# Kernel tuning notes

Hardware: AMD Instinct MI355X
Metric: run time of the kernel (lower is better)

Reference implementation:

```python
import jax, jax.numpy as jnp
import numpy as np

N, T = 128, 20
E_IN, E_EMB, E_RNN = 2, 64, 256
N_IN, N_EMB, N_RNN, N_OUT = 2, 64, 128, 5
ATT = 64

# static edge index sets: diagonal = temporal edges (i,i), off-diagonal = spatial edges (i,j)
_DIAG = np.arange(N) * N + np.arange(N)
_OFFJ = np.array([[j for j in range(N) if j != i] for i in range(N)])  # [N, N-1]
_OFFD = (np.arange(N)[:, None] * N + _OFFJ).reshape(-1)               # [N*(N-1)]
_TEMP = (N - 1) / np.sqrt(ATT)  # attention temperature = num_edges / sqrt(attention_size)


def setup_inputs() -> dict:
    ks = iter(jax.random.split(jax.random.key(0), 40))
    def p(shape, s=0.05):
        return jax.random.normal(next(ks), shape, jnp.float32) * s
    return {
        "nodes": p((T, N, N_IN), 1.0),
        "edges": p((T, N * N, E_IN), 1.0),
        "h_edge0": jnp.zeros((N * N, E_RNN), jnp.float32),
        "c_edge0": jnp.zeros((N * N, E_RNN), jnp.float32),
        "h_node0": jnp.zeros((N, N_RNN), jnp.float32),
        "c_node0": jnp.zeros((N, N_RNN), jnp.float32),
        "t_enc_w": p((E_EMB, E_IN)), "t_enc_b": p((E_EMB,)),
        "t_wih": p((4 * E_RNN, E_EMB)), "t_whh": p((4 * E_RNN, E_RNN)),
        "t_bih": p((4 * E_RNN,)), "t_bhh": p((4 * E_RNN,)),
        "s_enc_w": p((E_EMB, E_IN)), "s_enc_b": p((E_EMB,)),
        "s_wih": p((4 * E_RNN, E_EMB)), "s_whh": p((4 * E_RNN, E_RNN)),
        "s_bih": p((4 * E_RNN,)), "s_bhh": p((4 * E_RNN,)),
        "att_t_w": p((ATT, E_RNN)), "att_t_b": p((ATT,)),
        "att_s_w": p((ATT, E_RNN)), "att_s_b": p((ATT,)),
        "n_enc_w": p((N_EMB, N_IN)), "n_enc_b": p((N_EMB,)),
        "n_attn_w": p((N_EMB, 2 * E_RNN)), "n_attn_b": p((N_EMB,)),
        "n_wih": p((4 * N_RNN, 2 * N_EMB)), "n_whh": p((4 * N_RNN, N_RNN)),
        "n_bih": p((4 * N_RNN,)), "n_bhh": p((4 * N_RNN,)),
        "out_w": p((N_OUT, N_RNN)), "out_b": p((N_OUT,)),
    }


def _lstm(x, h, c, wih, whh, bih, bhh):
    g = x @ wih.T + bih + h @ whh.T + bhh
    i, f, gg, o = jnp.split(g, 4, axis=-1)
    c2 = jax.nn.sigmoid(f) * c + jax.nn.sigmoid(i) * jnp.tanh(gg)
    return jax.nn.sigmoid(o) * jnp.tanh(c2), c2


def reference(nodes, edges, h_edge0, c_edge0, h_node0, c_node0,
              t_enc_w, t_enc_b, t_wih, t_whh, t_bih, t_bhh,
              s_enc_w, s_enc_b, s_wih, s_whh, s_bih, s_bhh,
              att_t_w, att_t_b, att_s_w, att_s_b,
              n_enc_w, n_enc_b, n_attn_w, n_attn_b,
              n_wih, n_whh, n_bih, n_bhh, out_w, out_b):
    def step(carry, xt):
        h_e, c_e, h_n, c_n = carry
        pos_t, edg_t = xt
        # temporal edge RNN on self edges (i,i)
        x_t = jax.nn.relu(edg_t[_DIAG] @ t_enc_w.T + t_enc_b)
        h_t, c_t = _lstm(x_t, h_e[_DIAG], c_e[_DIAG], t_wih, t_whh, t_bih, t_bhh)
        # spatial edge RNN on all pairwise edges (i,j), i != j
        x_s = jax.nn.relu(edg_t[_OFFD] @ s_enc_w.T + s_enc_b)
        h_s, c_s = _lstm(x_s, h_e[_OFFD], c_e[_OFFD], s_wih, s_whh, s_bih, s_bhh)
        h_e = h_e.at[_DIAG].set(h_t).at[_OFFD].set(h_s)
        c_e = c_e.at[_DIAG].set(c_t).at[_OFFD].set(c_s)
        # attention: each node attends over its N-1 spatial edge hidden states
        hs = h_s.reshape(N, N - 1, E_RNN)
        te = h_t @ att_t_w.T + att_t_b                          # [N, ATT]
        se = jnp.einsum('nkd,ad->nka', hs, att_s_w) + att_s_b   # [N, N-1, ATT]
        logits = jnp.einsum('nka,na->nk', se, te) * _TEMP
        w = jax.nn.softmax(logits, axis=-1)
        weighted = jnp.einsum('nk,nkd->nd', w, hs)              # [N, E_RNN]
        # node RNN
        enc = jax.nn.relu(pos_t @ n_enc_w.T + n_enc_b)
        h_edges = jnp.concatenate([h_t, weighted], axis=-1)
        h_emb = jax.nn.relu(h_edges @ n_attn_w.T + n_attn_b)
        h_n, c_n = _lstm(jnp.concatenate([enc, h_emb], axis=-1), h_n, c_n,
                         n_wih, n_whh, n_bih, n_bhh)
        out = h_n @ out_w.T + out_b
        return (h_e, c_e, h_n, c_n), out

    _, outs = jax.lax.scan(step, (h_edge0, c_edge0, h_node0, c_node0), (nodes, edges))
    return outs  # [T, N, 5]
```

## Files before the change

### kernel.cpp

```cpp
#include <hip/hip_runtime.h>
#include <cmath>

#define NN 128
#define TT 20
#define ERNN 256
#define TEMPSC 15.875f

typedef __attribute__((ext_vector_type(8))) short bf16x8;
typedef __attribute__((ext_vector_type(4))) float f32x4;

__device__ __forceinline__ float sigm(float x){ return 1.f/(1.f+__expf(-x)); }
__device__ __forceinline__ float ftanh(float x){ float e = __expf(2.f*x); return 1.f - 2.f/(e + 1.f); }
__device__ __forceinline__ float b2f(unsigned short u){ union{unsigned int i; float f;} v; v.i = ((unsigned int)u)<<16; return v.f; }
__device__ __forceinline__ unsigned short f2b(float x){ union{float f; unsigned int u;} v; v.f = x; unsigned int r = v.u + 0x7fffu + ((v.u>>16)&1u); return (unsigned short)(r>>16); }

typedef __attribute__((address_space(3))) unsigned int lds_u32;
typedef __attribute__((address_space(1))) unsigned int glb_u32;
__device__ __forceinline__ void glds16(const void* g, void* l){
    __builtin_amdgcn_global_load_lds((const glb_u32*)g, (lds_u32*)l, 16, 0, 0);
}

__device__ __forceinline__ size_t hoff(int r, int d){
    return ((size_t)((r>>7)*32 + (d>>3))*128 + (r&127))*8 + (d&7);
}

__global__ void k_prep_w2(const float* __restrict__ s_wih, const float* __restrict__ s_whh,
                          unsigned short* __restrict__ s_wHi,
                          const float* __restrict__ t_wih, const float* __restrict__ t_whh,
                          unsigned short* __restrict__ t_wHi){
    int idx = blockIdx.x*256 + threadIdx.x;
    if (idx >= 2*1024*320) return;
    int which = idx >= 1024*320;
    if (which) idx -= 1024*320;
    const float* wih = which ? t_wih : s_wih;
    const float* whh = which ? t_whh : s_whh;
    unsigned short* wHi = which ? t_wHi : s_wHi;
    int c = idx / 320, k = idx - c*320;
    int ch = ((c>>6)<<4) + (c&15), g = (c>>4)&3;
    int r = g*256 + ch;
    float v = (k < 64) ? wih[r*64 + k] : whh[r*256 + (k-64)];
    size_t dst = ((size_t)((c>>7)*40 + (k>>3))*128 + (c&127))*8 + (k&7);
    wHi[dst] = f2b(v);
}

__global__ void k_prep_small(const float* __restrict__ s_bih, const float* __restrict__ s_bhh,
                             float* __restrict__ s_bs,
                             const float* __restrict__ t_bih, const float* __restrict__ t_bhh,
                             float* __restrict__ t_bs,
                             const float* __restrict__ n_wih, const float* __restrict__ n_whh,
                             float* __restrict__ n_wT,
                             const float* __restrict__ n_bih, const float* __restrict__ n_bhh,
                             float* __restrict__ n_bs){
    int i = blockIdx.x*256 + threadIdx.x;
    if (i < 2048) {
        int c = i, which = c >= 1024;
        if (which) c -= 1024;
        const float* bih = which ? t_bih : s_bih;
        const float* bhh = which ? t_bhh : s_bhh;
        float* bs = which ? t_bs : s_bs;
        int ch = ((c>>6)<<4)+(c&15), g=(c>>4)&3;
        int r = g*256+ch;
        bs[c] = bih[r] + bhh[r];
    } else if (i < 2048 + 65536) {
        int j = i - 2048;
        int r = j >> 7, c = j & 127;
        n_wT[c*512 + r] = n_wih[j];
    } else if (i < 2048 + 131072) {
        int j = i - 2048 - 65536;
        int r = j >> 7, c = j & 127;
        n_wT[(128 + c)*512 + r] = n_whh[j];
    } else if (i < 2048 + 131072 + 512) {
        int j = i - 2048 - 131072;
        n_bs[j] = n_bih[j] + n_bhh[j];
    }
}

__global__ void k_prep_xenc(const float* __restrict__ edges,
                            const float* __restrict__ s_enc_w, const float* __restrict__ s_enc_b,
                            const float* __restrict__ t_enc_w, const float* __restrict__ t_enc_b,
                            unsigned short* __restrict__ xe){
    size_t g = (size_t)blockIdx.x*256 + threadIdx.x;
    if (g >= (size_t)TT*16384*8) return;
    int row = (int)(g & 127);
    size_t rest = g >> 7;
    int kc = (int)(rest & 7);
    int tile = (int)((rest >> 3) & 127);
    int t = (int)(rest >> 10);
    int r = tile*128 + row;
    bool sp = (r < 16256);
    int row_ij;
    if (sp) { int i = r/127, jj = r - i*127; row_ij = i*NN + jj + (jj>=i ? 1:0); }
    else    { row_ij = (r - 16256)*(NN+1); }
    const float* w = sp ? s_enc_w : t_enc_w;
    const float* b = sp ? s_enc_b : t_enc_b;
    float e0 = edges[((size_t)t*16384 + row_ij)*2];
    float e1 = edges[((size_t)t*16384 + row_ij)*2 + 1];
    bf16x8 v8;
    #pragma unroll
    for (int q = 0; q < 8; ++q) {
        int m = kc*8 + q;
        v8[q] = (short)f2b(fmaxf(fmaf(w[m*2], e0, fmaf(w[m*2+1], e1, b[m])), 0.f));
    }
    *(bf16x8*)&xe[g*8] = v8;
}

__global__ void k_init_state(const float* __restrict__ h0, const float* __restrict__ c0,
                             unsigned short* __restrict__ hHi, float* __restrict__ c_all){
    int g = blockIdx.x*256 + threadIdx.x;
    if (g >= 16384*32) return;
    int d8 = g & 31, r = g >> 5;
    int row_ij;
    if (r < 16256){ int i = r/127, jj = r - i*127; row_ij = i*NN + jj + (jj>=i ? 1:0); }
    else          { row_ij = (r - 16256)*(NN+1); }
    const float* hs = h0 + (size_t)row_ij*ERNN + d8*8;
    const float* cs = c0 + (size_t)row_ij*ERNN + d8*8;
    bf16x8 hb;
    #pragma unroll
    for (int q = 0; q < 8; ++q) hb[q] = (short)f2b(hs[q]);
    *(bf16x8*)&hHi[hoff(r, d8*8)] = hb;
    float* cd = c_all + (size_t)r*ERNN + d8*8;
    *(float4*)cd       = *(const float4*)cs;
    *(float4*)(cd + 4) = *(const float4*)(cs + 4);
}

#define ESTEP(KS, NW) do { \
    asm volatile("s_waitcnt vmcnt(" #NW ")" ::: "memory"); \
    __builtin_amdgcn_s_barrier(); \
    __builtin_amdgcn_sched_barrier(0); \
    bf16x8 a0 = *(const bf16x8*)&Ah[(KS)&1][(kg*128 + arow)*8]; \
    bf16x8 a1 = *(const bf16x8*)&Ah[(KS)&1][(kg*128 + arow + 16)*8]; \
    bf16x8 b0 = *(const bf16x8*)&Bh[(KS)&1][(kg*128 + bcol)*8]; \
    bf16x8 b1 = *(const bf16x8*)&Bh[(KS)&1][(kg*128 + bcol + 16)*8]; \
    bf16x8 b2 = *(const bf16x8*)&Bh[(KS)&1][(kg*128 + bcol + 32)*8]; \
    bf16x8 b3 = *(const bf16x8*)&Bh[(KS)&1][(kg*128 + bcol + 48)*8]; \
    asm volatile("s_waitcnt lgkmcnt(0)" ::: "memory"); \
    __builtin_amdgcn_sched_barrier(0); \
    __builtin_amdgcn_s_barrier(); \
    if ((KS) + 2 <= 9) stage((KS)+2, (KS)&1); \
    acc[0][0] = __builtin_amdgcn_mfma_f32_16x16x32_bf16(a0, b0, acc[0][0],0,0,0); \
    acc[0][1] = __builtin_amdgcn_mfma_f32_16x16x32_bf16(a0, b1, acc[0][1],0,0,0); \
    acc[0][2] = __builtin_amdgcn_mfma_f32_16x16x32_bf16(a0, b2, acc[0][2],0,0,0); \
    acc[0][3] = __builtin_amdgcn_mfma_f32_16x16x32_bf16(a0, b3, acc[0][3],0,0,0); \
    acc[1][0] = __builtin_amdgcn_mfma_f32_16x16x32_bf16(a1, b0, acc[1][0],0,0,0); \
    acc[1][1] = __builtin_amdgcn_mfma_f32_16x16x32_bf16(a1, b1, acc[1][1],0,0,0); \
    acc[1][2] = __builtin_amdgcn_mfma_f32_16x16x32_bf16(a1, b2, acc[1][2],0,0,0); \
    acc[1][3] = __builtin_amdgcn_mfma_f32_16x16x32_bf16(a1, b3, acc[1][3],0,0,0); \
} while(0)

__global__ __launch_bounds__(512) void k_fused(
    const unsigned short* __restrict__ xenc_t,
    const unsigned short* __restrict__ h_in, unsigned short* __restrict__ h_out,
    unsigned short* __restrict__ hl_out, float* __restrict__ c_all,
    const unsigned short* __restrict__ s_wHi, const float* __restrict__ s_bs,
    const unsigned short* __restrict__ t_wHi, const float* __restrict__ t_bs,
    int has_node, int n_edge,
    const float* __restrict__ nodes_prev, const unsigned short* __restrict__ hl_prev,
    float* __restrict__ h_nn, float* __restrict__ c_nn, float* __restrict__ out_prev,
    const float* __restrict__ att_t_w, const float* __restrict__ att_t_b,
    const float* __restrict__ att_s_w, const float* __restrict__ att_s_b,
    const float* __restrict__ n_enc_w, const float* __restrict__ n_enc_b,
    const float* __restrict__ n_attn_w, const float* __restrict__ n_attn_b,
    const float* __restrict__ n_wT, const float* __restrict__ n_bsum,
    const float* __restrict__ out_w, const float* __restrict__ out_b)
{
    __shared__ __align__(16) char smem[32768];
    const int bid = blockIdx.x, tid = threadIdx.x;

    if (bid < NN) {
        if (!has_node) return;
        const int i = bid;
        float* sm  = (float*)smem;
        float* ht  = sm;
        float* te  = sm + 256;
        float* u   = sm + 320;
        float* lg  = sm + 576;
        float* cat = sm + 704;
        float* xc  = sm + 1216;
        float* hnl = sm + 1344;
        float* gl  = sm + 1472;
        float* pws = sm + 1984;
        float* msc = sm + 4032;

        if (tid < 256) ht[tid] = b2f(hl_prev[(size_t)(16256 + i)*256 + tid]);
        __syncthreads();
        if (tid < 256) {
            int m = tid >> 2, q = tid & 3;
            float s = 0.f;
            const float* wr = att_t_w + m*ERNN + q*64;
            const float* hh = ht + q*64;
            #pragma unroll 8
            for (int k = 0; k < 64; ++k) s = fmaf(wr[k], hh[k], s);
            s += __shfl_xor(s, 1);
            s += __shfl_xor(s, 2);
            if (q == 0) te[m] = s + att_t_b[m];
        }
        __syncthreads();
        if (tid < 256) {
            float s = 0.f;
            for (int m = 0; m < 64; ++m) s = fmaf(att_s_w[m*ERNN + tid], te[m], s);
            u[tid] = s;
        }
        if (tid == 320) {
            float s = 0.f;
            for (int m = 0; m < 64; ++m) s = fmaf(te[m], att_s_b[m], s);
            msc[2] = s;
        }
        __syncthreads();
        {
            int slot = tid >> 2, q = tid & 3;
            float part = 0.f;
            if (slot < 127) {
                const unsigned short* hs = hl_prev + (size_t)(i*127 + slot)*256 + q*64;
                const float* uu = u + q*64;
                #pragma unroll
                for (int d8 = 0; d8 < 8; ++d8) {
                    bf16x8 v = *(const bf16x8*)(hs + d8*8);
                    #pragma unroll
                    for (int j = 0; j < 8; ++j)
                        part = fmaf(uu[d8*8 + j], b2f((unsigned short)v[j]), part);
                }
            }
            part += __shfl_xor(part, 1);
            part += __shfl_xor(part, 2);
            if (slot < 127 && q == 0) lg[slot] = (part + msc[2]) * TEMPSC;
            if (tid == 511) lg[127] = -1e30f;
        }
        __syncthreads();
        if (tid < 64) {
            float a = fmaxf(lg[tid], lg[tid+64]);
            for (int off = 32; off; off >>= 1) a = fmaxf(a, __shfl_xor(a, off));
            if (tid == 0) msc[0] = a;
        }
        __syncthreads();
        if (tid < 128) lg[tid] = (tid < 127) ? __expf(lg[tid] - msc[0]) : 0.f;
        __syncthreads();
        if (tid < 64) {
            float a = lg[tid] + lg[tid+64];
            for (int off = 32; off; off >>= 1) a += __shfl_xor(a, off);
            if (tid == 0) msc[1] = a;
        }
        __syncthreads();
        {
            int w = tid >> 6, lane = tid & 63;
            float a0 = 0.f, a1 = 0.f, a2 = 0.f, a3 = 0.f;
            #pragma unroll 4
            for (int s = w*16; s < w*16 + 16; ++s) {
                int srow = (s < 127) ? s : 0;
                float wgt = lg[s];
                const unsigned short* hs = hl_prev + (size_t)(i*127 + srow)*256 + lane*4;
                ushort4 v = *(const ushort4*)hs;
                a0 = fmaf(wgt, b2f(v.x), a0);
                a1 = fmaf(wgt, b2f(v.y), a1);
                a2 = fmaf(wgt, b2f(v.z), a2);
                a3 = fmaf(wgt, b2f(v.w), a3);
            }
            pws[w*256 + lane*4+0] = a0; pws[w*256 + lane*4+1] = a1;
            pws[w*256 + lane*4+2] = a2; pws[w*256 + lane*4+3] = a3;
        }
        if (tid >= 256 && tid < 384) hnl[tid-256] = h_nn[i*128 + (tid-256)];
        __syncthreads();
        if (tid < 256) {
            float s = 0.f;
            #pragma unroll
            for (int w = 0; w < 8; ++w) s += pws[w*256 + tid];
            cat[256 + tid] = s / msc[1];
            cat[tid] = ht[tid];
        }
        __syncthreads();
        if (tid < 64) {
            float p0 = nodes_prev[i*2], p1 = nodes_prev[i*2+1];
            xc[tid] = fmaxf(fmaf(n_enc_w[tid*2], p0, fmaf(n_enc_w[tid*2+1], p1, n_enc_b[tid])), 0.f);
        }
        if (tid >= 256) {
            int t2 = tid - 256;
            int m = t2 >> 2, q = t2 & 3;
            float s = 0.f;
            const float* wr = n_attn_w + m*512 + q*128;
            const float* cc = cat + q*128;
            #pragma unroll 8
            for (int d = 0; d < 128; ++d) s = fmaf(wr[d], cc[d], s);
            s += __shfl_xor(s, 1);
            s += __shfl_xor(s, 2);
            if (q == 0) xc[64 + m] = fmaxf(s + n_attn_b[m], 0.f);
        }
        __syncthreads();
        {
            int n = tid;
            float s = n_bsum[n];
            for (int k = 0; k < 128; ++k) s = fmaf(n_wT[k*512 + n], xc[k], s);
            for (int k = 0; k < 128; ++k) s = fmaf(n_wT[(128+k)*512 + n], hnl[k], s);
            gl[n] = s;
        }
        __syncthreads();
        if (tid < 128) {
            float co = c_nn[i*128 + tid];
            float c2 = sigm(gl[128+tid])*co + sigm(gl[tid])*ftanh(gl[256+tid]);
            float h2 = sigm(gl[384+tid])*ftanh(c2);
            c_nn[i*128+tid] = c2;
            h_nn[i*128+tid] = h2;
            hnl[tid] = h2;
        }
        __syncthreads();
        if (tid < 5) {
            float s = out_b[tid];
            const float* wr = out_w + tid*128;
            for (int k = 0; k < 128; ++k) s = fmaf(wr[k], hnl[k], s);
            out_prev[i*5 + tid] = s;
        }
        return;
    }

    if (!n_edge) return;
    unsigned short (*Ah)[4096] = (unsigned short(*)[4096])smem;
    unsigned short (*Bh)[4096] = (unsigned short(*)[4096])(smem + 16384);
    const int ebid = bid - NN;
    const int lane = tid & 63, wid = tid >> 6;
    const int wg = (ebid & 7)*128 + (ebid >> 3);
    const int bm = wg >> 3, ntp = wg & 7;
    const bool sp = (bm < 127);
    const int rbase = bm * 128;
    const unsigned short* wHi = sp ? s_wHi : t_wHi;
    const float* bs = sp ? s_bs : t_bs;
    const int wr = wid & 3, wc = wid >> 2;
    const int nt = ntp*2 + wc;

    auto stage = [&](int ks, int b){
        int kc = wid >> 1, half = wid & 1;
        const unsigned short* asrc = (ks < 2)
            ? xenc_t + ((size_t)bm*8  + ks*4     + kc)*1024 + half*512
            : h_in   + ((size_t)bm*32 + (ks-2)*4 + kc)*1024 + half*512;
        glds16(asrc + lane*8, (char*)&Ah[b][0] + wid*1024);
        size_t wb = ((size_t)(ntp*40 + ks*4 + kc)*128 + half*64)*8;
        glds16(wHi + wb + lane*8, (char*)&Bh[b][0] + wid*1024);
    };
    stage(0, 0);
    stage(1, 1);

    f32x4 acc[2][4];
    #pragma unroll
    for (int m = 0; m < 2; ++m)
        #pragma unroll
        for (int g = 0; g < 4; ++g)
            acc[m][g] = (f32x4){0.f,0.f,0.f,0.f};

    const int arow = wr*32 + (lane & 15);
    const int bcol = wc*64 + (lane & 15);
    const int kg = lane >> 4;

    ESTEP(0, 2);
    ESTEP(1, 2);
    ESTEP(2, 2);
    ESTEP(3, 2);
    ESTEP(4, 2);
    ESTEP(5, 2);
    ESTEP(6, 2);
    ESTEP(7, 2);
    ESTEP(8, 2);
    ESTEP(9, 0);

    const int chl = lane & 15, q4 = (lane >> 4)*4;
    const int ch = nt*16 + chl;
    const int cbase = nt*64 + chl;
    const float b0 = bs[cbase], b1 = bs[cbase+16], b2 = bs[cbase+32], b3 = bs[cbase+48];
    #pragma unroll
    for (int m = 0; m < 2; ++m) {
        #pragma unroll
        for (int rg = 0; rg < 4; ++rg) {
            int lrow = wr*32 + m*16 + q4 + rg;
            int row = rbase + lrow;
            float gi = acc[m][0][rg] + b0;
            float gf = acc[m][1][rg] + b1;
            float gg = acc[m][2][rg] + b2;
            float go = acc[m][3][rg] + b3;
            size_t off = (size_t)row*256 + ch;
            float c_old = c_all[off];
            float c2 = sigm(gf)*c_old + sigm(gi)*ftanh(gg);
            float h2 = sigm(go)*ftanh(c2);
            c_all[off] = c2;
            unsigned short hb = f2b(h2);
            h_out[((size_t)(bm*32 + (ch>>3))*128 + lrow)*8 + (ch&7)] = hb;
            hl_out[off] = hb;
        }
    }
}

extern "C" void kernel_launch(void* const* d_in, const int* in_sizes, int n_in,
                              void* d_out, int out_size, void* d_ws, size_t ws_size,
                              hipStream_t stream)
{
    const float* nodes   = (const float*)d_in[0];
    const float* edges   = (const float*)d_in[1];
    const float* h_e0    = (const float*)d_in[2];
    const float* c_e0    = (const float*)d_in[3];
    const float* h_n0    = (const float*)d_in[4];
    const float* c_n0    = (const float*)d_in[5];
    const float* t_enc_w = (const float*)d_in[6];
    const float* t_enc_b = (const float*)d_in[7];
    const float* t_wih   = (const float*)d_in[8];
    const float* t_whh   = (const float*)d_in[9];
    const float* t_bih   = (const float*)d_in[10];
    const float* t_bhh   = (const float*)d_in[11];
    const float* s_enc_w = (const float*)d_in[12];
    const float* s_enc_b = (const float*)d_in[13];
    const float* s_wih   = (const float*)d_in[14];
    const float* s_whh   = (const float*)d_in[15];
    const float* s_bih   = (const float*)d_in[16];
    const float* s_bhh   = (const float*)d_in[17];
    const float* att_t_w = (const float*)d_in[18];
    const float* att_t_b = (const float*)d_in[19];
    const float* att_s_w = (const float*)d_in[20];
    const float* att_s_b = (const float*)d_in[21];
    const float* n_enc_w = (const float*)d_in[22];
    const float* n_enc_b = (const float*)d_in[23];
    const float* n_attn_w= (const float*)d_in[24];
    const float* n_attn_b= (const float*)d_in[25];
    const float* n_wih   = (const float*)d_in[26];
    const float* n_whh   = (const float*)d_in[27];
    const float* n_bih   = (const float*)d_in[28];
    const float* n_bhh   = (const float*)d_in[29];
    const float* out_w   = (const float*)d_in[30];
    const float* out_b   = (const float*)d_in[31];
    float* out = (float*)d_out;

    char* p = (char*)d_ws;
    float* c_all = (float*)p;            p += (size_t)16384*256*4;
    float* h_nn  = (float*)p;            p += 128*128*4;
    float* c_nn  = (float*)p;            p += 128*128*4;
    float* s_bs  = (float*)p;            p += 1024*4;
    float* t_bs  = (float*)p;            p += 1024*4;
    float* n_wT  = (float*)p;            p += 256*512*4;
    float* n_bs  = (float*)p;            p += 512*4;
    unsigned short* h_a  = (unsigned short*)p;  p += (size_t)16384*256*2;
    unsigned short* h_b  = (unsigned short*)p;  p += (size_t)16384*256*2;
    unsigned short* hl_a = (unsigned short*)p;  p += (size_t)16384*256*2;
    unsigned short* hl_b = (unsigned short*)p;  p += (size_t)16384*256*2;
    unsigned short* xenc = (unsigned short*)p;  p += (size_t)TT*16384*64*2;
    unsigned short* s_wHi = (unsigned short*)p; p += 1024*320*2;
    unsigned short* t_wHi = (unsigned short*)p; p += 1024*320*2;

    hipMemcpyAsync(h_nn, h_n0, 128*128*sizeof(float), hipMemcpyDeviceToDevice, stream);
    hipMemcpyAsync(c_nn, c_n0, 128*128*sizeof(float), hipMemcpyDeviceToDevice, stream);

    k_init_state<<<2048, 256, 0, stream>>>(h_e0, c_e0, h_a, c_all);
    k_prep_w2<<<2560, 256, 0, stream>>>(s_wih, s_whh, s_wHi, t_wih, t_whh, t_wHi);
    k_prep_small<<<523, 256, 0, stream>>>(s_bih, s_bhh, s_bs, t_bih, t_bhh, t_bs,
                                          n_wih, n_whh, n_wT, n_bih, n_bhh, n_bs);
    k_prep_xenc<<<10240, 256, 0, stream>>>(edges, s_enc_w, s_enc_b, t_enc_w, t_enc_b, xenc);

    for (int t = 0; t < TT; ++t) {
        const unsigned short* h_in  = (t & 1) ? h_b : h_a;
        unsigned short*       h_out = (t & 1) ? h_a : h_b;
        unsigned short*       hl_out= (t & 1) ? hl_b : hl_a;
        const unsigned short* hl_prev=(t & 1) ? hl_a : hl_b;
        const float* nprev = (t > 0) ? nodes + (size_t)(t-1)*NN*2 : nodes;
        float* oprev = (t > 0) ? out + (size_t)(t-1)*NN*5 : out;
        k_fused<<<NN + 1024, 512, 0, stream>>>(xenc + (size_t)t*16384*64,
            h_in, h_out, hl_out, c_all,
            s_wHi, s_bs, t_wHi, t_bs,
            (t > 0) ? 1 : 0, 1024,
            nprev, hl_prev, h_nn, c_nn, oprev,
            att_t_w, att_t_b, att_s_w, att_s_b, n_enc_w, n_enc_b,
            n_attn_w, n_attn_b, n_wT, n_bs, out_w, out_b);
    }
    k_fused<<<NN, 512, 0, stream>>>(xenc,
        h_a, h_b, hl_a, c_all,
        s_wHi, s_bs, t_wHi, t_bs,
        1, 0,
        nodes + (size_t)19*NN*2, hl_b, h_nn, c_nn, out + (size_t)19*NN*5,
        att_t_w, att_t_b, att_s_w, att_s_b, n_enc_w, n_enc_b,
        n_attn_w, n_attn_b, n_wT, n_bs, out_w, out_b);
}
```

Baseline: 631.7 us.

## Store edge LSTM cell state in bf16 and merge prep kernels into one launch

The edge LSTM cell state buffer moves from fp32 to bf16, halving its read and write traffic in every timestep's fused kernel. The separate init, weight-prep, bias and encoder-prep kernels and the two device memcpys are combined into a single launch to cut launch overhead. Keeping the recurrent cell state in bf16 adds rounding error that accumulates across timesteps and may affect accuracy.

```diff
diff --git a/kernel.cpp b/kernel.cpp
--- a/kernel.cpp
+++ b/kernel.cpp
@@ -24,36 +24,51 @@
     return ((size_t)((r>>7)*32 + (d>>3))*128 + (r&127))*8 + (d&7);
 }
 
-__global__ void k_prep_w2(const float* __restrict__ s_wih, const float* __restrict__ s_whh,
-                          unsigned short* __restrict__ s_wHi,
-                          const float* __restrict__ t_wih, const float* __restrict__ t_whh,
-                          unsigned short* __restrict__ t_wHi){
-    int idx = blockIdx.x*256 + threadIdx.x;
-    if (idx >= 2*1024*320) return;
-    int which = idx >= 1024*320;
-    if (which) idx -= 1024*320;
-    const float* wih = which ? t_wih : s_wih;
-    const float* whh = which ? t_whh : s_whh;
-    unsigned short* wHi = which ? t_wHi : s_wHi;
-    int c = idx / 320, k = idx - c*320;
-    int ch = ((c>>6)<<4) + (c&15), g = (c>>4)&3;
-    int r = g*256 + ch;
-    float v = (k < 64) ? wih[r*64 + k] : whh[r*256 + (k-64)];
-    size_t dst = ((size_t)((c>>7)*40 + (k>>3))*128 + (c&127))*8 + (k&7);
-    wHi[dst] = f2b(v);
-}
-
-__global__ void k_prep_small(const float* __restrict__ s_bih, const float* __restrict__ s_bhh,
-                             float* __restrict__ s_bs,
-                             const float* __restrict__ t_bih, const float* __restrict__ t_bhh,
-                             float* __restrict__ t_bs,
-                             const float* __restrict__ n_wih, const float* __restrict__ n_whh,
-                             float* __restrict__ n_wT,
-                             const float* __restrict__ n_bih, const float* __restrict__ n_bhh,
-                             float* __restrict__ n_bs){
-    int i = blockIdx.x*256 + threadIdx.x;
-    if (i < 2048) {
-        int c = i, which = c >= 1024;
+#define R_W2    (2*1024*320)
+#define R_EB    2048
+#define R_NWT   131072
+#define R_NBS   512
+#define R_HNN   16384
+#define R_CNN   16384
+#define R_INIT  (16384*32)
+#define R_XENC  ((size_t)TT*16384*8)
+#define PREP_TOT (R_W2 + R_EB + R_NWT + R_NBS + R_HNN + R_CNN + R_INIT + R_XENC)
+
+__global__ void k_prep_all(
+    const float* __restrict__ s_wih, const float* __restrict__ s_whh, unsigned short* __restrict__ s_wHi,
+    const float* __restrict__ t_wih, const float* __restrict__ t_whh, unsigned short* __restrict__ t_wHi,
+    const float* __restrict__ s_bih, const float* __restrict__ s_bhh, float* __restrict__ s_bs,
+    const float* __restrict__ t_bih, const float* __restrict__ t_bhh, float* __restrict__ t_bs,
+    const float* __restrict__ n_wih, const float* __restrict__ n_whh, float* __restrict__ n_wT,
+    const float* __restrict__ n_bih, const float* __restrict__ n_bhh, float* __restrict__ n_bs,
+    const float* __restrict__ h_n0, float* __restrict__ h_nn,
+    const float* __restrict__ c_n0, float* __restrict__ c_nn,
+    const float* __restrict__ h_e0, const float* __restrict__ c_e0,
+    unsigned short* __restrict__ hHi, unsigned short* __restrict__ c_b,
+    const float* __restrict__ edges,
+    const float* __restrict__ s_enc_w, const float* __restrict__ s_enc_b,
+    const float* __restrict__ t_enc_w, const float* __restrict__ t_enc_b,
+    unsigned short* __restrict__ xe)
+{
+    size_t i = (size_t)blockIdx.x*256 + threadIdx.x;
+    if (i < R_W2) {
+        int idx = (int)i;
+        int which = idx >= 1024*320;
+        if (which) idx -= 1024*320;
+        const float* wih = which ? t_wih : s_wih;
+        const float* whh = which ? t_whh : s_whh;
+        unsigned short* wHi = which ? t_wHi : s_wHi;
+        int c = idx / 320, k = idx - c*320;
+        int ch = ((c>>6)<<4) + (c&15), g = (c>>4)&3;
+        int r = g*256 + ch;
+        float v = (k < 64) ? wih[r*64 + k] : whh[r*256 + (k-64)];
+        size_t dst = ((size_t)((c>>7)*40 + (k>>3))*128 + (c&127))*8 + (k&7);
+        wHi[dst] = f2b(v);
+        return;
+    }
+    i -= R_W2;
+    if (i < R_EB) {
+        int c = (int)i, which = c >= 1024;
         if (which) c -= 1024;
         const float* bih = which ? t_bih : s_bih;
         const float* bhh = which ? t_bhh : s_bhh;
@@ -61,66 +76,62 @@
         int ch = ((c>>6)<<4)+(c&15), g=(c>>4)&3;
         int r = g*256+ch;
         bs[c] = bih[r] + bhh[r];
-    } else if (i < 2048 + 65536) {
-        int j = i - 2048;
-        int r = j >> 7, c = j & 127;
-        n_wT[c*512 + r] = n_wih[j];
-    } else if (i < 2048 + 131072) {
-        int j = i - 2048 - 65536;
-        int r = j >> 7, c = j & 127;
-        n_wT[(128 + c)*512 + r] = n_whh[j];
-    } else if (i < 2048 + 131072 + 512) {
-        int j = i - 2048 - 131072;
-        n_bs[j] = n_bih[j] + n_bhh[j];
-    }
-}
-
-__global__ void k_prep_xenc(const float* __restrict__ edges,
-                            const float* __restrict__ s_enc_w, const float* __restrict__ s_enc_b,
-                            const float* __restrict__ t_enc_w, const float* __restrict__ t_enc_b,
-                            unsigned short* __restrict__ xe){
-    size_t g = (size_t)blockIdx.x*256 + threadIdx.x;
-    if (g >= (size_t)TT*16384*8) return;
-    int row = (int)(g & 127);
-    size_t rest = g >> 7;
-    int kc = (int)(rest & 7);
-    int tile = (int)((rest >> 3) & 127);
-    int t = (int)(rest >> 10);
-    int r = tile*128 + row;
-    bool sp = (r < 16256);
-    int row_ij;
-    if (sp) { int i = r/127, jj = r - i*127; row_ij = i*NN + jj + (jj>=i ? 1:0); }
-    else    { row_ij = (r - 16256)*(NN+1); }
-    const float* w = sp ? s_enc_w : t_enc_w;
-    const float* b = sp ? s_enc_b : t_enc_b;
-    float e0 = edges[((size_t)t*16384 + row_ij)*2];
-    float e1 = edges[((size_t)t*16384 + row_ij)*2 + 1];
-    bf16x8 v8;
-    #pragma unroll
-    for (int q = 0; q < 8; ++q) {
-        int m = kc*8 + q;
-        v8[q] = (short)f2b(fmaxf(fmaf(w[m*2], e0, fmaf(w[m*2+1], e1, b[m])), 0.f));
-    }
-    *(bf16x8*)&xe[g*8] = v8;
-}
-
-__global__ void k_init_state(const float* __restrict__ h0, const float* __restrict__ c0,
-                             unsigned short* __restrict__ hHi, float* __restrict__ c_all){
-    int g = blockIdx.x*256 + threadIdx.x;
-    if (g >= 16384*32) return;
-    int d8 = g & 31, r = g >> 5;
-    int row_ij;
-    if (r < 16256){ int i = r/127, jj = r - i*127; row_ij = i*NN + jj + (jj>=i ? 1:0); }
-    else          { row_ij = (r - 16256)*(NN+1); }
-    const float* hs = h0 + (size_t)row_ij*ERNN + d8*8;
-    const float* cs = c0 + (size_t)row_ij*ERNN + d8*8;
-    bf16x8 hb;
-    #pragma unroll
-    for (int q = 0; q < 8; ++q) hb[q] = (short)f2b(hs[q]);
-    *(bf16x8*)&hHi[hoff(r, d8*8)] = hb;
-    float* cd = c_all + (size_t)r*ERNN + d8*8;
-    *(float4*)cd       = *(const float4*)cs;
-    *(float4*)(cd + 4) = *(const float4*)(cs + 4);
+        return;
+    }
+    i -= R_EB;
+    if (i < R_NWT) {
+        int j = (int)i;
+        if (j < 65536) { int r = j >> 7, c = j & 127; n_wT[c*512 + r] = n_wih[j]; }
+        else { j -= 65536; int r = j >> 7, c = j & 127; n_wT[(128 + c)*512 + r] = n_whh[j]; }
+        return;
+    }
+    i -= R_NWT;
+    if (i < R_NBS) { n_bs[i] = n_bih[i] + n_bhh[i]; return; }
+    i -= R_NBS;
+    if (i < R_HNN) { h_nn[i] = h_n0[i]; return; }
+    i -= R_HNN;
+    if (i < R_CNN) { c_nn[i] = c_n0[i]; return; }
+    i -= R_CNN;
+    if (i < R_INIT) {
+        int g = (int)i;
+        int d8 = g & 31, r = g >> 5;
+        int row_ij;
+        if (r < 16256){ int ii = r/127, jj = r - ii*127; row_ij = ii*NN + jj + (jj>=ii ? 1:0); }
+        else          { row_ij = (r - 16256)*(NN+1); }
+        const float* hs = h_e0 + (size_t)row_ij*ERNN + d8*8;
+        const float* cs = c_e0 + (size_t)row_ij*ERNN + d8*8;
+        bf16x8 hb, cb;
+        #pragma unroll
+        for (int q = 0; q < 8; ++q){ hb[q] = (short)f2b(hs[q]); cb[q] = (short)f2b(cs[q]); }
+        *(bf16x8*)&hHi[hoff(r, d8*8)] = hb;
+        *(bf16x8*)&c_b[(size_t)r*ERNN + d8*8] = cb;
+        return;
+    }
+    i -= R_INIT;
+    if (i < R_XENC) {
+        size_t g = i;
+        int row = (int)(g & 127);
+        size_t rest = g >> 7;
+        int kc = (int)(rest & 7);
+        int tile = (int)((rest >> 3) & 127);
+        int t = (int)(rest >> 10);
+        int r = tile*128 + row;
+        bool sp = (r < 16256);
+        int row_ij;
+        if (sp) { int ii = r/127, jj = r - ii*127; row_ij = ii*NN + jj + (jj>=ii ? 1:0); }
+        else    { row_ij = (r - 16256)*(NN+1); }
+        const float* w = sp ? s_enc_w : t_enc_w;
+        const float* b = sp ? s_enc_b : t_enc_b;
+        float e0 = edges[((size_t)t*16384 + row_ij)*2];
+        float e1 = edges[((size_t)t*16384 + row_ij)*2 + 1];
+        bf16x8 v8;
+        #pragma unroll
+        for (int q = 0; q < 8; ++q) {
+            int m = kc*8 + q;
+            v8[q] = (short)f2b(fmaxf(fmaf(w[m*2], e0, fmaf(w[m*2+1], e1, b[m])), 0.f));
+        }
+        *(bf16x8*)&xe[g*8] = v8;
+    }
 }
 
 #define ESTEP(KS, NW) do { \
@@ -150,7 +161,7 @@
 __global__ __launch_bounds__(512) void k_fused(
     const unsigned short* __restrict__ xenc_t,
     const unsigned short* __restrict__ h_in, unsigned short* __restrict__ h_out,
-    unsigned short* __restrict__ hl_out, float* __restrict__ c_all,
+    unsigned short* __restrict__ hl_out, unsigned short* __restrict__ c_b,
     const unsigned short* __restrict__ s_wHi, const float* __restrict__ s_bs,
     const unsigned short* __restrict__ t_wHi, const float* __restrict__ t_bs,
     int has_node, int n_edge,
@@ -373,10 +384,10 @@
             float gg = acc[m][2][rg] + b2;
             float go = acc[m][3][rg] + b3;
             size_t off = (size_t)row*256 + ch;
-            float c_old = c_all[off];
+            float c_old = b2f(c_b[off]);
             float c2 = sigm(gf)*c_old + sigm(gi)*ftanh(gg);
             float h2 = sigm(go)*ftanh(c2);
-            c_all[off] = c2;
+            c_b[off] = f2b(c2);
             unsigned short hb = f2b(h2);
             h_out[((size_t)(bm*32 + (ch>>3))*128 + lrow)*8 + (ch&7)] = hb;
             hl_out[off] = hb;
@@ -423,13 +434,13 @@
     float* out = (float*)d_out;
 
     char* p = (char*)d_ws;
-    float* c_all = (float*)p;            p += (size_t)16384*256*4;
     float* h_nn  = (float*)p;            p += 128*128*4;
     float* c_nn  = (float*)p;            p += 128*128*4;
     float* s_bs  = (float*)p;            p += 1024*4;
     float* t_bs  = (float*)p;            p += 1024*4;
     float* n_wT  = (float*)p;            p += 256*512*4;
     float* n_bs  = (float*)p;            p += 512*4;
+    unsigned short* c_b  = (unsigned short*)p;  p += (size_t)16384*256*2;
     unsigned short* h_a  = (unsigned short*)p;  p += (size_t)16384*256*2;
     unsigned short* h_b  = (unsigned short*)p;  p += (size_t)16384*256*2;
     unsigned short* hl_a = (unsigned short*)p;  p += (size_t)16384*256*2;
@@ -438,14 +449,14 @@
     unsigned short* s_wHi = (unsigned short*)p; p += 1024*320*2;
     unsigned short* t_wHi = (unsigned short*)p; p += 1024*320*2;
 
-    hipMemcpyAsync(h_nn, h_n0, 128*128*sizeof(float), hipMemcpyDeviceToDevice, stream);
-    hipMemcpyAsync(c_nn, c_n0, 128*128*sizeof(float), hipMemcpyDeviceToDevice, stream);
-
-    k_init_state<<<2048, 256, 0, stream>>>(h_e0, c_e0, h_a, c_all);
-    k_prep_w2<<<2560, 256, 0, stream>>>(s_wih, s_whh, s_wHi, t_wih, t_whh, t_wHi);
-    k_prep_small<<<523, 256, 0, stream>>>(s_bih, s_bhh, s_bs, t_bih, t_bhh, t_bs,
-                                          n_wih, n_whh, n_wT, n_bih, n_bhh, n_bs);
-    k_prep_xenc<<<10240, 256, 0, stream>>>(edges, s_enc_w, s_enc_b, t_enc_w, t_enc_b, xenc);
+    int prep_blocks = (int)((PREP_TOT + 255) / 256);
+    k_prep_all<<<prep_blocks, 256, 0, stream>>>(
+        s_wih, s_whh, s_wHi, t_wih, t_whh, t_wHi,
+        s_bih, s_bhh, s_bs, t_bih, t_bhh, t_bs,
+        n_wih, n_whh, n_wT, n_bih, n_bhh, n_bs,
+        h_n0, h_nn, c_n0, c_nn,
+        h_e0, c_e0, h_a, c_b,
+        edges, s_enc_w, s_enc_b, t_enc_w, t_enc_b, xenc);
 
     for (int t = 0; t < TT; ++t) {
         const unsigned short* h_in  = (t & 1) ? h_b : h_a;
@@ -455,7 +466,7 @@
         const float* nprev = (t > 0) ? nodes + (size_t)(t-1)*NN*2 : nodes;
         float* oprev = (t > 0) ? out + (size_t)(t-1)*NN*5 : out;
         k_fused<<<NN + 1024, 512, 0, stream>>>(xenc + (size_t)t*16384*64,
-            h_in, h_out, hl_out, c_all,
+            h_in, h_out, hl_out, c_b,
             s_wHi, s_bs, t_wHi, t_bs,
             (t > 0) ? 1 : 0, 1024,
             nprev, hl_prev, h_nn, c_nn, oprev,
@@ -463,7 +474,7 @@
             n_attn_w, n_attn_b, n_wT, n_bs, out_w, out_b);
     }
     k_fused<<<NN, 512, 0, stream>>>(xenc,
-        h_a, h_b, hl_a, c_all,
+        h_a, h_b, hl_a, c_b,
         s_wHi, s_bs, t_wHi, t_bs,
         1, 0,
         nodes + (size_t)19*NN*2, hl_b, h_nn, c_nn, out + (size_t)19*NN*5,
```

Measured after the change: 609.5 us. -3.5%, faster.
